# Optimization experiments

Measured on AMD Instinct MI355X. Metric: run time of the kernel, lower is better.

The kernel has to match this reference:

```python
import jax, jax.numpy as jnp
import numpy as np
from jax.scipy.special import logsumexp

K = 50
EPSILON = 1e-3
N_ITERS = 100


def setup_inputs() -> dict:
    key = jax.random.key(0)
    scores = jax.random.normal(key, (16, 512), dtype=jnp.float32)
    return {"scores": scores}


def reference(scores):
    # scores: [B, n]
    scores_sorted = -jnp.sort(-scores, axis=-1)  # descending sort, [B, n]
    # cost[b, i, j] = (scores[b, i] - scores_sorted[b, j])**2  -> [B, n, n]
    cost = (scores[:, :, None] - scores_sorted[:, None, :]) ** 2
    log_P0 = -cost / EPSILON

    def sinkhorn_step(log_P, _):
        log_P = log_P - logsumexp(log_P, axis=-2, keepdims=True)  # column normalize
        log_P = log_P - logsumexp(log_P, axis=-1, keepdims=True)  # row normalize
        return log_P, None

    log_P, _ = jax.lax.scan(sinkhorn_step, log_P0, None, length=N_ITERS)
    soft_permutation = jnp.exp(log_P)  # [B, n, n]
    # probability of being among top-k: sum over first k columns of the soft permutation
    top_k_probs = jnp.sum(soft_permutation[:, :, :K], axis=-1)  # [B, n]
    return top_k_probs
```

## Files before the change

### kernel.cpp

```cpp
#include <hip/hip_runtime.h>


#define N      512
#define BATCH  16
#define KTOP   50
#define NAPPS  30
#define NJ     11
#define COEF   1442.6950408889634f
#define ONEH2  0x3C003C00u
#define NT     256
#define XPAD   5
#define XLEN   (256 + 2 * XPAD)

typedef _Float16 h2 __attribute__((ext_vector_type(2)));

static __device__ __forceinline__ h2 pack2(float a, float b) {
    return __builtin_bit_cast(h2, __builtin_amdgcn_cvt_pkrtz(a, b));
}
static __device__ __forceinline__ h2 uh(unsigned v) {
    return __builtin_bit_cast(h2, v);
}

__global__
__attribute__((amdgpu_flat_work_group_size(NT, NT)))
void sinkhorn_topk_kernel(const float* __restrict__ scores,
                          float* __restrict__ out) {
    __shared__ __align__(16) float tv[N];
    __shared__ int                 ti[N];
    __shared__ unsigned            xb[2][XLEN];

    const int g = threadIdx.x;
    const int b = blockIdx.x;

    ((float2*)tv)[g] = ((const float2*)(scores + b * N))[g];
    ti[2 * g]     = 2 * g;
    ti[2 * g + 1] = 2 * g + 1;
    if (g < XPAD) {
        xb[0][g] = 0u;            xb[1][g] = 0u;
        xb[0][XLEN - 1 - g] = 0u; xb[1][XLEN - 1 - g] = 0u;
    }
    xb[0][XPAD + g] = ONEH2;
    __syncthreads();

    for (int k = 2; k <= N; k <<= 1) {
        for (int j = k >> 1; j > 0; j >>= 1) {
            int i = ((g & ~(j - 1)) << 1) | (g & (j - 1));
            int p = i | j;
            float va = tv[i], vb = tv[p];
            bool up = ((i & k) == 0);
            bool sw = up ? (va < vb) : (va > vb);
            if (sw) {
                tv[i] = vb; tv[p] = va;
                int t_ = ti[i]; ti[i] = ti[p]; ti[p] = t_;
            }
            __syncthreads();
        }
    }

    const int gb = 2 * g - 10;
    const float t0 = tv[2 * g], t1 = tv[2 * g + 1];
    h2 K2[2][NJ];
#pragma unroll
    for (int d = 0; d < NJ; ++d) {
        int g0 = gb + 2 * d, g1 = g0 + 1;
        int c0 = min(max(g0, 0), N - 1), c1 = min(max(g1, 0), N - 1);
        float s0 = tv[c0], s1 = tv[c1];
        float d00 = t0 - s0, d01 = t0 - s1;
        float d10 = t1 - s0, d11 = t1 - s1;
        K2[0][d] = pack2(exp2f(-COEF * d00 * d00), exp2f(-COEF * d01 * d01));
        K2[1][d] = pack2(exp2f(-COEF * d10 * d10), exp2f(-COEF * d11 * d11));
    }

    unsigned w[NJ];
    unsigned x = ONEH2;

    auto run_app = [&](const unsigned* rb, unsigned* wb) {
#pragma unroll
        for (int d = 0; d < NJ; ++d)
            if (d != 5) w[d] = rb[g + d];
        w[5] = x;
        float a0 = __builtin_amdgcn_fdot2(K2[0][0], uh(w[0]), 0.f, false);
        float a1 = __builtin_amdgcn_fdot2(K2[1][0], uh(w[0]), 0.f, false);
        float b0 = __builtin_amdgcn_fdot2(K2[0][1], uh(w[1]), 0.f, false);
        float b1 = __builtin_amdgcn_fdot2(K2[1][1], uh(w[1]), 0.f, false);
#pragma unroll
        for (int d = 2; d < NJ; d += 2) {
            a0 = __builtin_amdgcn_fdot2(K2[0][d], uh(w[d]), a0, false);
            a1 = __builtin_amdgcn_fdot2(K2[1][d], uh(w[d]), a1, false);
            if (d + 1 < NJ) {
                b0 = __builtin_amdgcn_fdot2(K2[0][d + 1], uh(w[d + 1]), b0, false);
                b1 = __builtin_amdgcn_fdot2(K2[1][d + 1], uh(w[d + 1]), b1, false);
            }
        }
        float s0 = a0 + b0, s1 = a1 + b1;
        x = __builtin_bit_cast(unsigned,
                pack2(__builtin_amdgcn_rcpf(s0), __builtin_amdgcn_rcpf(s1)));
        if (wb) {
            wb[XPAD + g] = x;
            __syncthreads();
        }
    };

    unsigned* B0 = &xb[0][0];
    unsigned* B1 = &xb[1][0];
#pragma unroll 1
    for (int it = 0; it < (NAPPS - 2) / 2; ++it) {
        run_app(B0, B1);
        run_app(B1, B0);
    }
    run_app(B0, B1);
    run_app(B1, nullptr);

    unsigned cmask[NJ];
#pragma unroll
    for (int d = 0; d < NJ; ++d) {
        int g0 = gb + 2 * d, g1 = g0 + 1;
        h2 cw = uh(w[d]);
        float c0 = (g0 >= 0 && g0 < KTOP) ? (float)cw[0] : 0.f;
        float c1 = (g1 >= 0 && g1 < KTOP) ? (float)cw[1] : 0.f;
        cmask[d] = __builtin_bit_cast(unsigned, pack2(c0, c1));
    }
    float k0 = 0.f, k1 = 0.f;
#pragma unroll
    for (int d = 0; d < NJ; ++d) {
        k0 = __builtin_amdgcn_fdot2(K2[0][d], uh(cmask[d]), k0, false);
        k1 = __builtin_amdgcn_fdot2(K2[1][d], uh(cmask[d]), k1, false);
    }
    h2 xr = uh(x);
    out[b * N + ti[2 * g]]     = (float)xr[0] * k0;
    out[b * N + ti[2 * g + 1]] = (float)xr[1] * k1;
}

extern "C" void kernel_launch(void* const* d_in, const int* in_sizes, int n_in,
                              void* d_out, int out_size, void* d_ws, size_t ws_size,
                              hipStream_t stream) {
    const float* scores = (const float*)d_in[0];
    float* out = (float*)d_out;
    sinkhorn_topk_kernel<<<dim3(BATCH), dim3(NT), 0, stream>>>(scores, out);
}
```

Before: 65.13 us.

## Move bitonic sort into registers with wavefront shuffles, minimizing barriers

The bitonic sort now keeps two values and indices per thread in registers. Intra-thread stages use selects, strides within a 64-lane wavefront use shuffles, and only strides that cross wavefronts go through shared memory with barriers. This removes most of the per-stage __syncthreads and LDS traffic in the sort phase. The sort is only part of a kernel dominated by the Sinkhorn iterations, so the overall effect depends on how much time the sort took.

```diff
diff --git a/kernel.cpp b/kernel.cpp
--- a/kernel.cpp
+++ b/kernel.cpp
@@ -26,15 +26,16 @@
 void sinkhorn_topk_kernel(const float* __restrict__ scores,
                           float* __restrict__ out) {
     __shared__ __align__(16) float tv[N];
-    __shared__ int                 ti[N];
+    __shared__ __align__(16) int   ti[N];
     __shared__ unsigned            xb[2][XLEN];
 
     const int g = threadIdx.x;
     const int b = blockIdx.x;
 
-    ((float2*)tv)[g] = ((const float2*)(scores + b * N))[g];
-    ti[2 * g]     = 2 * g;
-    ti[2 * g + 1] = 2 * g + 1;
+    float2 s2 = ((const float2*)(scores + b * N))[g];
+    float v0 = s2.x, v1 = s2.y;
+    int   i0 = 2 * g, i1 = 2 * g + 1;
+
     if (g < XPAD) {
         xb[0][g] = 0u;            xb[1][g] = 0u;
         xb[0][XLEN - 1 - g] = 0u; xb[1][XLEN - 1 - g] = 0u;
@@ -42,23 +43,53 @@
     xb[0][XPAD + g] = ONEH2;
     __syncthreads();
 
+#pragma unroll
     for (int k = 2; k <= N; k <<= 1) {
+#pragma unroll
         for (int j = k >> 1; j > 0; j >>= 1) {
-            int i = ((g & ~(j - 1)) << 1) | (g & (j - 1));
-            int p = i | j;
-            float va = tv[i], vb = tv[p];
-            bool up = ((i & k) == 0);
-            bool sw = up ? (va < vb) : (va > vb);
-            if (sw) {
-                tv[i] = vb; tv[p] = va;
-                int t_ = ti[i]; ti[i] = ti[p]; ti[p] = t_;
+            if (j == 1) {
+                bool desc = ((g & (k >> 1)) == 0);
+                bool c = desc ? (v1 > v0) : (v1 < v0);
+                float tf = v0; int tix = i0;
+                v0 = c ? v1 : v0;  i0 = c ? i1 : i0;
+                v1 = c ? tf : v1;  i1 = c ? tix : i1;
+            } else if (j < 128) {
+                const int m = j >> 1;
+                float pv0 = __shfl_xor(v0, m, 64);
+                float pv1 = __shfl_xor(v1, m, 64);
+                int   pi0 = __shfl_xor(i0, m, 64);
+                int   pi1 = __shfl_xor(i1, m, 64);
+                bool flip = (((g & (k >> 1)) != 0) ^ ((g & m) != 0));
+                bool c0 = flip ? (pv0 < v0) : (pv0 > v0);
+                bool c1 = flip ? (pv1 < v1) : (pv1 > v1);
+                v0 = c0 ? pv0 : v0; i0 = c0 ? pi0 : i0;
+                v1 = c1 ? pv1 : v1; i1 = c1 ? pi1 : i1;
+            } else {
+                const int m = j >> 1;
+                float2 t2; t2.x = v0; t2.y = v1;
+                int2   o2; o2.x = i0; o2.y = i1;
+                ((float2*)tv)[g] = t2;
+                ((int2*)ti)[g]   = o2;
+                __syncthreads();
+                float2 p2 = ((float2*)tv)[g ^ m];
+                int2   q2 = ((int2*)ti)[g ^ m];
+                bool flip = (((g & (k >> 1)) != 0) ^ ((g & m) != 0));
+                bool c0 = flip ? (p2.x < v0) : (p2.x > v0);
+                bool c1 = flip ? (p2.y < v1) : (p2.y > v1);
+                v0 = c0 ? p2.x : v0; i0 = c0 ? q2.x : i0;
+                v1 = c1 ? p2.y : v1; i1 = c1 ? q2.y : i1;
+                __syncthreads();
             }
-            __syncthreads();
         }
     }
+    {
+        float2 t2; t2.x = v0; t2.y = v1;
+        ((float2*)tv)[g] = t2;
+    }
+    __syncthreads();
 
     const int gb = 2 * g - 10;
-    const float t0 = tv[2 * g], t1 = tv[2 * g + 1];
+    const float t0 = v0, t1 = v1;
     h2 K2[2][NJ];
 #pragma unroll
     for (int d = 0; d < NJ; ++d) {
@@ -127,8 +158,8 @@
         k1 = __builtin_amdgcn_fdot2(K2[1][d], uh(cmask[d]), k1, false);
     }
     h2 xr = uh(x);
-    out[b * N + ti[2 * g]]     = (float)xr[0] * k0;
-    out[b * N + ti[2 * g + 1]] = (float)xr[1] * k1;
+    out[b * N + i0] = (float)xr[0] * k0;
+    out[b * N + i1] = (float)xr[1] * k1;
 }
 
 extern "C" void kernel_launch(void* const* d_in, const int* in_sizes, int n_in,
```

After: 64.20 us. Within noise of the previous version (-1.4%).
